# Kernel optimization log

Measured on AMD Instinct MI355X. Metric: run time of the kernel, lower is better.

## Reference

```python
import jax, jax.numpy as jnp
import numpy as np

# dims: channels=512, kernel_size=1, stride=1
B, N, D = 8, 4096, 512
G, GC = 32, 16          # involution groups = D // 16, group_channels = 16
RED = D // 4            # involution reduction_ratio = 4
HID = int(D * 0.25) + 1 # CondConv attention hidden = int(in_planes*0.25)+1 = 129
K = 4                   # number of dynamic-conv experts
TEMP = 34.0             # CondConv softmax temperature
EPS = 1e-5


def setup_inputs() -> dict:
    key = jax.random.key(0)
    ks = jax.random.split(key, 6)
    sc = lambda k, shape, fan: jax.random.normal(k, shape, jnp.float32) / np.float32(np.sqrt(fan))
    return {
        "x": jax.random.normal(ks[0], (B, N, D), jnp.float32),
        # involution: 1x1 conv D->RED (no bias), eval-mode BN, 1x1 conv RED->G (k^2*groups with k=1)
        "conv1_w": sc(ks[1], (RED, D), D),
        "bn_gamma": jnp.ones((RED,), jnp.float32),
        "bn_beta": jnp.zeros((RED,), jnp.float32),
        "bn_mean": jnp.zeros((RED,), jnp.float32),
        "bn_var": jnp.ones((RED,), jnp.float32),
        "conv2_w": sc(ks[2], (G, RED), RED),
        "conv2_b": jnp.zeros((G,), jnp.float32),
        # Dynamic_conv1d (CondConv): attention MLP + K expert 1x1 kernels [K, out, in]
        "fc1_w": sc(ks[3], (HID, D), D),
        "fc2_w": sc(ks[4], (K, HID), HID),
        "fc2_b": jnp.zeros((K,), jnp.float32),
        "dyn_w": sc(ks[5], (K, D, D), D),
        "dyn_b": jnp.zeros((K, D), jnp.float32),
        # LayerNorm(channels)
        "ln_gamma": jnp.ones((D,), jnp.float32),
        "ln_beta": jnp.zeros((D,), jnp.float32),
    }


def reference(x, conv1_w, bn_gamma, bn_beta, bn_mean, bn_var, conv2_w, conv2_b,
              fc1_w, fc2_w, fc2_b, dyn_w, dyn_b, ln_gamma, ln_beta):
    b, n, d = x.shape
    # --- involution branch (k=1, stride=1): per-position, per-group scalar gating ---
    h = jnp.einsum('bnd,rd->bnr', x, conv1_w)                       # 1x1 conv
    h = (h - bn_mean) / jnp.sqrt(bn_var + EPS) * bn_gamma + bn_beta # eval BN
    h = jax.nn.relu(h)
    gate = jnp.einsum('bnr,gr->bng', h, conv2_w) + conv2_b          # [b,n,G] kernel weights (k^2=1)
    out1 = (x.reshape(b, n, G, GC) * gate[..., None]).reshape(b, n, d)
    # --- CondConv dynamic conv1d branch (k=1) ---
    pooled = x.mean(axis=1)                                          # adaptive avg pool over length -> [b,d]
    a = jax.nn.relu(pooled @ fc1_w.T)                                # [b,HID]
    att = jax.nn.softmax((a @ fc2_w.T + fc2_b) / TEMP, axis=-1)      # [b,K]
    Wb = jnp.einsum('bk,kod->bod', att, dyn_w)                       # per-sample kernel [b,d,d]
    bb = att @ dyn_b                                                 # [b,d]
    out2 = jnp.einsum('bnd,bod->bno', x, Wb) + bb[:, None, :]
    # --- LayerNorm + double residual ---
    y = out1 + out2
    mu = y.mean(-1, keepdims=True)
    var = y.var(-1, keepdims=True)
    y = (y - mu) / jnp.sqrt(var + EPS) * ln_gamma + ln_beta
    return y + x
```

## Files before the change

### kernel.cpp

```cpp
#include <hip/hip_runtime.h>

#define DI __device__ __forceinline__

typedef __bf16 bf8 __attribute__((ext_vector_type(8)));
typedef float f4 __attribute__((ext_vector_type(4)));
typedef unsigned short us4 __attribute__((ext_vector_type(4)));
typedef unsigned short us8 __attribute__((ext_vector_type(8)));

#define BB 8
#define NN 4096
#define DD 512
#define RED 128
#define GG 32
#define HID 129

DI float b2f(unsigned short u) {
    union { unsigned int i; float f; } c; c.i = ((unsigned int)u) << 16; return c.f;
}
DI unsigned short f2b(float f) {
    union { float f; unsigned int i; } c; c.f = f;
    unsigned int u = c.i;
    return (unsigned short)((u + 0x7fffu + ((u >> 16) & 1u)) >> 16);
}

typedef const __attribute__((address_space(1))) void* gp1_t;
typedef __attribute__((address_space(3))) void* lp3_t;
DI void gld16(const void* g, void* l) {
    __builtin_amdgcn_global_load_lds((gp1_t)g, (lp3_t)l, 16, 0, 0);
}

__global__ __launch_bounds__(256) void kpre(const float* __restrict__ x,
                                            const float* __restrict__ conv1_w,
                                            const float* __restrict__ conv2_w,
                                            float* __restrict__ part,
                                            unsigned short* __restrict__ xb,
                                            unsigned short* __restrict__ c1b,
                                            unsigned short* __restrict__ c2b) {
    int c = blockIdx.x, b = blockIdx.y, t = threadIdx.x;
    __shared__ float red[2][512];
    if (c >= 128) {
        int idx = ((c - 128) * 8 + b) * 256 + t;
        if (idx < 16384) {
            size_t off = (size_t)idx * 4;
            float4 v = *(const float4*)(conv1_w + off);
            us4 o; o[0] = f2b(v.x); o[1] = f2b(v.y); o[2] = f2b(v.z); o[3] = f2b(v.w);
            *(us4*)(c1b + off) = o;
        } else if (idx < 17408) {
            size_t off = (size_t)(idx - 16384) * 4;
            float4 v = *(const float4*)(conv2_w + off);
            us4 o; o[0] = f2b(v.x); o[1] = f2b(v.y); o[2] = f2b(v.z); o[3] = f2b(v.w);
            *(us4*)(c2b + off) = o;
        }
        return;
    }
    int rg = t >> 7, cg = t & 127;
    int row0 = c * 32 + rg * 16;
    float4 s = {0.f, 0.f, 0.f, 0.f};
#pragma unroll 4
    for (int i = 0; i < 16; ++i) {
        size_t off = ((size_t)(b * NN + row0 + i) * DD) + cg * 4;
        float4 v = *(const float4*)(x + off);
        s.x += v.x; s.y += v.y; s.z += v.z; s.w += v.w;
        us4 o; o[0] = f2b(v.x); o[1] = f2b(v.y); o[2] = f2b(v.z); o[3] = f2b(v.w);
        *(us4*)(xb + off) = o;
    }
    *(float4*)&red[rg][cg * 4] = s;
    __syncthreads();
    if (t < 128) {
        float4 aa = *(const float4*)&red[0][t * 4];
        float4 bb4 = *(const float4*)&red[1][t * 4];
        float4 o;
        o.x = aa.x + bb4.x; o.y = aa.y + bb4.y;
        o.z = aa.z + bb4.z; o.w = aa.w + bb4.w;
        *(float4*)(part + (size_t)(b * 128 + c) * DD + t * 4) = o;
    }
}

__global__ __launch_bounds__(256, 3) void kgate(
    const unsigned short* __restrict__ xb, const unsigned short* __restrict__ c1b,
    const float* __restrict__ bn_g, const float* __restrict__ bn_b,
    const float* __restrict__ bn_m, const float* __restrict__ bn_v,
    const unsigned short* __restrict__ c2b, const float* __restrict__ conv2_b,
    float* __restrict__ gate) {
    int bid = blockIdx.x;
    int b = bid & 7, mtile = bid >> 3;
    int row0 = mtile * 128;
    int t = threadIdx.x;
    int w = t >> 6, lane = t & 63, q = lane >> 4, l16 = lane & 15;
    int wr = (w & 1) * 64, wc = (w >> 1) * 64;

    __shared__ unsigned short As[4096], Bs[4096];
    __shared__ unsigned short h_s[128][136];
    __shared__ float bnS[RED], bnT[RED];

    if (t < RED) {
        float sc = bn_g[t] * rsqrtf(bn_v[t] + 1e-5f);
        bnS[t] = sc;
        bnT[t] = bn_b[t] - bn_m[t] * sc;
    }

    f4 acc[4][4];
#pragma unroll
    for (int mi = 0; mi < 4; ++mi)
#pragma unroll
        for (int ni = 0; ni < 4; ++ni) acc[mi][ni] = (f4){0.f, 0.f, 0.f, 0.f};

    const unsigned short* abase = xb + ((size_t)(b * NN + row0) * DD);
    const int r1 = t >> 2, k1 = (t & 3) * 8;
    const int r2 = 64 + r1, k2 = k1;
    unsigned short* As1 = &As[(size_t)w * 512];
    unsigned short* As2 = &As[2048 + (size_t)w * 512];
    unsigned short* Bs1 = &Bs[(size_t)w * 512];
    unsigned short* Bs2 = &Bs[2048 + (size_t)w * 512];

    for (int ks = 0; ks < 16; ++ks) {
        __syncthreads();
        int kk = ks * 32;
        gld16(abase + (size_t)r1 * DD + kk + k1, As1);
        gld16(abase + (size_t)r2 * DD + kk + k2, As2);
        gld16(c1b + (size_t)r1 * DD + kk + k1, Bs1);
        gld16(c1b + (size_t)r2 * DD + kk + k2, Bs2);
        __syncthreads();
        bf8 af[4], bv[4];
#pragma unroll
        for (int mi = 0; mi < 4; ++mi) af[mi] = *(const bf8*)&As[(wr + mi * 16 + l16) * 32 + q * 8];
#pragma unroll
        for (int ni = 0; ni < 4; ++ni) bv[ni] = *(const bf8*)&Bs[(wc + ni * 16 + l16) * 32 + q * 8];
#pragma unroll
        for (int ni = 0; ni < 4; ++ni)
#pragma unroll
            for (int mi = 0; mi < 4; ++mi)
                acc[mi][ni] = __builtin_amdgcn_mfma_f32_16x16x32_bf16(af[mi], bv[ni], acc[mi][ni], 0, 0, 0);
    }
    __syncthreads();
#pragma unroll
    for (int ni = 0; ni < 4; ++ni) {
        int hc = wc + ni * 16 + l16;
        float sc = bnS[hc], sh = bnT[hc];
#pragma unroll
        for (int mi = 0; mi < 4; ++mi)
#pragma unroll
            for (int r = 0; r < 4; ++r) {
                int row = wr + mi * 16 + q * 4 + r;
                h_s[row][hc] = f2b(fmaxf(acc[mi][ni][r] * sc + sh, 0.f));
            }
    }
    __syncthreads();
    f4 a2[2][2];
#pragma unroll
    for (int mi = 0; mi < 2; ++mi)
#pragma unroll
        for (int ni = 0; ni < 2; ++ni) a2[mi][ni] = (f4){0.f, 0.f, 0.f, 0.f};
#pragma unroll
    for (int ks = 0; ks < 4; ++ks) {
        bf8 ah[2], bh[2];
#pragma unroll
        for (int mi = 0; mi < 2; ++mi)
            ah[mi] = *(const bf8*)&h_s[w * 32 + mi * 16 + l16][ks * 32 + q * 8];
#pragma unroll
        for (int ni = 0; ni < 2; ++ni)
            bh[ni] = *(const bf8*)(c2b + (ni * 16 + l16) * RED + ks * 32 + q * 8);
#pragma unroll
        for (int ni = 0; ni < 2; ++ni)
#pragma unroll
            for (int mi = 0; mi < 2; ++mi)
                a2[mi][ni] = __builtin_amdgcn_mfma_f32_16x16x32_bf16(ah[mi], bh[ni], a2[mi][ni], 0, 0, 0);
    }
#pragma unroll
    for (int ni = 0; ni < 2; ++ni) {
        int g = ni * 16 + l16;
        float cb = conv2_b[g];
#pragma unroll
        for (int mi = 0; mi < 2; ++mi)
#pragma unroll
            for (int r = 0; r < 4; ++r) {
                int row = w * 32 + mi * 16 + q * 4 + r;
                gate[((size_t)(b * NN + row0 + row)) * GG + g] = a2[mi][ni][r] + cb;
            }
    }
}

__global__ __launch_bounds__(256) void katt(const float* __restrict__ part,
                                            const float* __restrict__ fc1_w,
                                            const float* __restrict__ fc2_w,
                                            const float* __restrict__ fc2_b,
                                            const float* __restrict__ dyn_b,
                                            float* __restrict__ att, float* __restrict__ bb) {
    int b = blockIdx.x, t = threadIdx.x;
    __shared__ float sh[2][512];
    __shared__ float pooled[512];
    __shared__ float a_s[HID + 3];
    __shared__ float att_s[4];
    {
        int cg = t & 127, half = t >> 7;
        const float* pb = part + ((size_t)b * 128 + half * 64) * DD + cg * 4;
        float4 s = {0.f, 0.f, 0.f, 0.f};
#pragma unroll 8
        for (int r = 0; r < 64; ++r) {
            float4 v = *(const float4*)(pb + (size_t)r * DD);
            s.x += v.x; s.y += v.y; s.z += v.z; s.w += v.w;
        }
        *(float4*)&sh[half][cg * 4] = s;
    }
    __syncthreads();
    if (t < 128) {
        float4 aa = *(const float4*)&sh[0][t * 4];
        float4 bb4 = *(const float4*)&sh[1][t * 4];
        float4 o;
        o.x = (aa.x + bb4.x) * (1.0f / (float)NN);
        o.y = (aa.y + bb4.y) * (1.0f / (float)NN);
        o.z = (aa.z + bb4.z) * (1.0f / (float)NN);
        o.w = (aa.w + bb4.w) * (1.0f / (float)NN);
        *(float4*)&pooled[t * 4] = o;
    }
    __syncthreads();
    int wv = t >> 6, ln = t & 63;
    float pl[8];
    {
        float4 p0 = *(const float4*)&pooled[ln * 8];
        float4 p1 = *(const float4*)&pooled[ln * 8 + 4];
        pl[0] = p0.x; pl[1] = p0.y; pl[2] = p0.z; pl[3] = p0.w;
        pl[4] = p1.x; pl[5] = p1.y; pl[6] = p1.z; pl[7] = p1.w;
    }
    for (int jb = wv * 4; jb < 128; jb += 16) {
        float s4[4];
#pragma unroll
        for (int u = 0; u < 4; ++u) {
            const float* wr = fc1_w + (size_t)(jb + u) * DD + ln * 8;
            float4 w0 = *(const float4*)wr;
            float4 w1 = *(const float4*)(wr + 4);
            s4[u] = w0.x * pl[0] + w0.y * pl[1] + w0.z * pl[2] + w0.w * pl[3] +
                    w1.x * pl[4] + w1.y * pl[5] + w1.z * pl[6] + w1.w * pl[7];
        }
#pragma unroll
        for (int u = 0; u < 4; ++u) {
            float v = s4[u];
#pragma unroll
            for (int off = 32; off >= 1; off >>= 1) v += __shfl_xor(v, off);
            if (ln == 0) a_s[jb + u] = fmaxf(v, 0.f);
        }
    }
    if (wv == 0) {
        const float* wr = fc1_w + (size_t)128 * DD + ln * 8;
        float4 w0 = *(const float4*)wr;
        float4 w1 = *(const float4*)(wr + 4);
        float v = w0.x * pl[0] + w0.y * pl[1] + w0.z * pl[2] + w0.w * pl[3] +
                  w1.x * pl[4] + w1.y * pl[5] + w1.z * pl[6] + w1.w * pl[7];
#pragma unroll
        for (int off = 32; off >= 1; off >>= 1) v += __shfl_xor(v, off);
        if (ln == 0) a_s[128] = fmaxf(v, 0.f);
    }
    __syncthreads();
    {
        float v = 0.f;
        for (int j = ln; j < HID; j += 64) v += a_s[j] * fc2_w[wv * HID + j];
#pragma unroll
        for (int off = 32; off >= 1; off >>= 1) v += __shfl_xor(v, off);
        if (ln == 0) att_s[wv] = (v + fc2_b[wv]) * (1.0f / 34.0f);
    }
    __syncthreads();
    if (t == 0) {
        float lg[4], mx = -1e30f;
#pragma unroll
        for (int k = 0; k < 4; ++k) { lg[k] = att_s[k]; mx = fmaxf(mx, lg[k]); }
        float den = 0.f;
#pragma unroll
        for (int k = 0; k < 4; ++k) { lg[k] = __expf(lg[k] - mx); den += lg[k]; }
#pragma unroll
        for (int k = 0; k < 4; ++k) {
            float a = lg[k] / den;
            att_s[k] = a; att[b * 4 + k] = a;
        }
    }
    __syncthreads();
    float a0 = att_s[0], a1 = att_s[1], a2 = att_s[2], a3 = att_s[3];
    for (int o = t; o < DD; o += 256) {
        bb[b * DD + o] = a0 * dyn_b[o] + a1 * dyn_b[DD + o] +
                         a2 * dyn_b[2 * DD + o] + a3 * dyn_b[3 * DD + o];
    }
}

__global__ __launch_bounds__(256) void kwb(const float* __restrict__ dyn_w,
                                           const float* __restrict__ att,
                                           unsigned short* __restrict__ Wb) {
    int g = blockIdx.x * 256 + threadIdx.x;
    size_t pos = (size_t)g * 4;
    float4 w0 = *(const float4*)(dyn_w + pos);
    float4 w1 = *(const float4*)(dyn_w + 262144 + pos);
    float4 w2 = *(const float4*)(dyn_w + 524288 + pos);
    float4 w3 = *(const float4*)(dyn_w + 786432 + pos);
#pragma unroll
    for (int b = 0; b < 8; ++b) {
        float a0 = att[b * 4 + 0], a1 = att[b * 4 + 1], a2 = att[b * 4 + 2], a3 = att[b * 4 + 3];
        us4 o;
        o[0] = f2b(a0 * w0.x + a1 * w1.x + a2 * w2.x + a3 * w3.x);
        o[1] = f2b(a0 * w0.y + a1 * w1.y + a2 * w2.y + a3 * w3.y);
        o[2] = f2b(a0 * w0.z + a1 * w1.z + a2 * w2.z + a3 * w3.z);
        o[3] = f2b(a0 * w0.w + a1 * w1.w + a2 * w2.w + a3 * w3.w);
        *(us4*)(Wb + (size_t)b * 262144 + pos) = o;
    }
}

__global__ __launch_bounds__(256, 3) void kgemm(
    const unsigned short* __restrict__ xb, const unsigned short* __restrict__ Wb,
    const float* __restrict__ bb, float* __restrict__ out) {
    int bid = blockIdx.x;
    int b = bid & 7, tile = bid >> 3;
    int ntile = tile & 3, mtile = tile >> 2;
    int row0 = mtile * 128, col0 = ntile * 128;
    int t = threadIdx.x;
    int w = t >> 6, lane = t & 63, q = lane >> 4, l16 = lane & 15;
    int wr = (w & 1) * 64, wc = (w >> 1) * 64;

    __shared__ unsigned short As[4096], Bs[4096];

    f4 acc[4][4];
#pragma unroll
    for (int mi = 0; mi < 4; ++mi)
#pragma unroll
        for (int ni = 0; ni < 4; ++ni) acc[mi][ni] = (f4){0.f, 0.f, 0.f, 0.f};

    const unsigned short* abase = xb + ((size_t)(b * NN + row0) * DD);
    const unsigned short* bbase = Wb + ((size_t)(b * DD + col0)) * DD;
    const int r1 = t >> 2, k1 = (t & 3) * 8;
    const int r2 = 64 + r1;
    unsigned short* As1 = &As[(size_t)w * 512];
    unsigned short* As2 = &As[2048 + (size_t)w * 512];
    unsigned short* Bs1 = &Bs[(size_t)w * 512];
    unsigned short* Bs2 = &Bs[2048 + (size_t)w * 512];

    for (int ks = 0; ks < 16; ++ks) {
        __syncthreads();
        int kk = ks * 32;
        gld16(abase + (size_t)r1 * DD + kk + k1, As1);
        gld16(abase + (size_t)r2 * DD + kk + k1, As2);
        gld16(bbase + (size_t)r1 * DD + kk + k1, Bs1);
        gld16(bbase + (size_t)r2 * DD + kk + k1, Bs2);
        __syncthreads();
        bf8 af[4], bv[4];
#pragma unroll
        for (int mi = 0; mi < 4; ++mi) af[mi] = *(const bf8*)&As[(wr + mi * 16 + l16) * 32 + q * 8];
#pragma unroll
        for (int ni = 0; ni < 4; ++ni) bv[ni] = *(const bf8*)&Bs[(wc + ni * 16 + l16) * 32 + q * 8];
#pragma unroll
        for (int ni = 0; ni < 4; ++ni)
#pragma unroll
            for (int mi = 0; mi < 4; ++mi)
                acc[mi][ni] = __builtin_amdgcn_mfma_f32_16x16x32_bf16(af[mi], bv[ni], acc[mi][ni], 0, 0, 0);
    }
    const float* bbp = bb + b * DD + col0;
#pragma unroll
    for (int ni = 0; ni < 4; ++ni) {
        int col = wc + ni * 16 + l16;
        float bbv = bbp[col];
#pragma unroll
        for (int mi = 0; mi < 4; ++mi)
#pragma unroll
            for (int r = 0; r < 4; ++r) {
                int row = wr + mi * 16 + q * 4 + r;
                out[((size_t)(b * NN + row0 + row)) * DD + col0 + col] = acc[mi][ni][r] + bbv;
            }
    }
}

__global__ __launch_bounds__(256) void kln(const unsigned short* __restrict__ xb,
                                           const float* __restrict__ gate,
                                           const float* __restrict__ lnG,
                                           const float* __restrict__ lnB,
                                           float* __restrict__ out) {
    int t = threadIdx.x;
    int w = t >> 6, lane = t & 63;
    int rid = blockIdx.x * 4 + w;
    size_t base = (size_t)rid * DD + lane * 8;
    float4 y0 = *(const float4*)(out + base);
    float4 y1 = *(const float4*)(out + base + 4);
    us8 xv8 = *(const us8*)(xb + base);
    float g = gate[(size_t)rid * GG + (lane >> 1)];
    float xv[8], y[8];
#pragma unroll
    for (int i = 0; i < 8; ++i) xv[i] = b2f(xv8[i]);
    y[0] = y0.x + xv[0] * g; y[1] = y0.y + xv[1] * g;
    y[2] = y0.z + xv[2] * g; y[3] = y0.w + xv[3] * g;
    y[4] = y1.x + xv[4] * g; y[5] = y1.y + xv[5] * g;
    y[6] = y1.z + xv[6] * g; y[7] = y1.w + xv[7] * g;
    float s = 0.f, sq = 0.f;
#pragma unroll
    for (int i = 0; i < 8; ++i) { s += y[i]; sq += y[i] * y[i]; }
#pragma unroll
    for (int off = 32; off >= 1; off >>= 1) {
        s += __shfl_xor(s, off);
        sq += __shfl_xor(sq, off);
    }
    float mu = s * (1.f / 512.f);
    float rs = rsqrtf(sq * (1.f / 512.f) - mu * mu + 1e-5f);
    float4 g0 = *(const float4*)(lnG + lane * 8);
    float4 g1 = *(const float4*)(lnG + lane * 8 + 4);
    float4 b0 = *(const float4*)(lnB + lane * 8);
    float4 b1 = *(const float4*)(lnB + lane * 8 + 4);
    float lg[8] = {g0.x, g0.y, g0.z, g0.w, g1.x, g1.y, g1.z, g1.w};
    float lb[8] = {b0.x, b0.y, b0.z, b0.w, b1.x, b1.y, b1.z, b1.w};
    float4 o0, o1;
    o0.x = (y[0] - mu) * rs * lg[0] + lb[0] + xv[0];
    o0.y = (y[1] - mu) * rs * lg[1] + lb[1] + xv[1];
    o0.z = (y[2] - mu) * rs * lg[2] + lb[2] + xv[2];
    o0.w = (y[3] - mu) * rs * lg[3] + lb[3] + xv[3];
    o1.x = (y[4] - mu) * rs * lg[4] + lb[4] + xv[4];
    o1.y = (y[5] - mu) * rs * lg[5] + lb[5] + xv[5];
    o1.z = (y[6] - mu) * rs * lg[6] + lb[6] + xv[6];
    o1.w = (y[7] - mu) * rs * lg[7] + lb[7] + xv[7];
    *(float4*)(out + base) = o0;
    *(float4*)(out + base + 4) = o1;
}

extern "C" void kernel_launch(void* const* d_in, const int* in_sizes, int n_in,
                              void* d_out, int out_size, void* d_ws, size_t ws_size,
                              hipStream_t stream) {
    const float* x       = (const float*)d_in[0];
    const float* conv1_w = (const float*)d_in[1];
    const float* bn_g    = (const float*)d_in[2];
    const float* bn_b    = (const float*)d_in[3];
    const float* bn_m    = (const float*)d_in[4];
    const float* bn_v    = (const float*)d_in[5];
    const float* conv2_w = (const float*)d_in[6];
    const float* conv2_b = (const float*)d_in[7];
    const float* fc1_w   = (const float*)d_in[8];
    const float* fc2_w   = (const float*)d_in[9];
    const float* fc2_b   = (const float*)d_in[10];
    const float* dyn_w   = (const float*)d_in[11];
    const float* dyn_b   = (const float*)d_in[12];
    const float* lnG     = (const float*)d_in[13];
    const float* lnB     = (const float*)d_in[14];
    float* out = (float*)d_out;

    char* ws = (char*)d_ws;
    unsigned short* xb   = (unsigned short*)ws;
    float* part          = (float*)(ws + 33554432);
    float* att           = (float*)(ws + 37748736);
    float* bbw           = (float*)(ws + 37748864);
    unsigned short* c1b  = (unsigned short*)(ws + 37765248);
    unsigned short* c2b  = (unsigned short*)(ws + 37896320);
    float* gate          = (float*)(ws + 37904512);
    unsigned short* Wb   = (unsigned short*)(ws + 42098816);

    kpre<<<dim3(137, 8), 256, 0, stream>>>(x, conv1_w, conv2_w, part, xb, c1b, c2b);
    kgate<<<256, 256, 0, stream>>>(xb, c1b, bn_g, bn_b, bn_m, bn_v, c2b, conv2_b, gate);
    katt<<<8, 256, 0, stream>>>(part, fc1_w, fc2_w, fc2_b, dyn_b, att, bbw);
    kwb<<<256, 256, 0, stream>>>(dyn_w, att, Wb);
    kgemm<<<1024, 256, 0, stream>>>(xb, Wb, bbw, out);
    kln<<<8192, 256, 0, stream>>>(xb, gate, lnG, lnB, out);
}
```

Measured before the change: 231.5 us.

## Fuse dynamic-conv GEMM with gating and LayerNorm epilogue in one kernel

```diff
diff --git a/kernel.cpp b/kernel.cpp
--- a/kernel.cpp
+++ b/kernel.cpp
@@ -301,115 +301,136 @@
     }
 }
 
-__global__ __launch_bounds__(256, 3) void kgemm(
+#define STG_BUF 36864
+__global__ __launch_bounds__(512, 2) void kfuse(
     const unsigned short* __restrict__ xb, const unsigned short* __restrict__ Wb,
-    const float* __restrict__ bb, float* __restrict__ out) {
+    const float* __restrict__ bb, const float* __restrict__ gate,
+    const float* __restrict__ lnG, const float* __restrict__ lnB,
+    float* __restrict__ out) {
     int bid = blockIdx.x;
-    int b = bid & 7, tile = bid >> 3;
-    int ntile = tile & 3, mtile = tile >> 2;
-    int row0 = mtile * 128, col0 = ntile * 128;
+    int b = bid & 7, mtile = bid >> 3;
+    int row0 = mtile * 64;
     int t = threadIdx.x;
     int w = t >> 6, lane = t & 63, q = lane >> 4, l16 = lane & 15;
-    int wr = (w & 1) * 64, wc = (w >> 1) * 64;
-
-    __shared__ unsigned short As[4096], Bs[4096];
-
-    f4 acc[4][4];
-#pragma unroll
-    for (int mi = 0; mi < 4; ++mi)
-#pragma unroll
-        for (int ni = 0; ni < 4; ++ni) acc[mi][ni] = (f4){0.f, 0.f, 0.f, 0.f};
+    int wrow = (w >> 2) * 32, wcol = (w & 3) * 128;
+
+    __shared__ __align__(16) char smem[84480];
+    float* gateS = (float*)(smem + 73728);
+    float2* redS = (float2*)(smem + 81920);
+    float2* murs = (float2*)(smem + 83968);
 
     const unsigned short* abase = xb + ((size_t)(b * NN + row0) * DD);
-    const unsigned short* bbase = Wb + ((size_t)(b * DD + col0)) * DD;
-    const int r1 = t >> 2, k1 = (t & 3) * 8;
-    const int r2 = 64 + r1;
-    unsigned short* As1 = &As[(size_t)w * 512];
-    unsigned short* As2 = &As[2048 + (size_t)w * 512];
-    unsigned short* Bs1 = &Bs[(size_t)w * 512];
-    unsigned short* Bs2 = &Bs[2048 + (size_t)w * 512];
-
+    const unsigned short* wbase = Wb + ((size_t)b * DD) * DD;
+
+    {
+        int grow = t >> 3, gcol = (t & 7) * 4;
+        *(float4*)&gateS[t * 4] =
+            *(const float4*)(gate + ((size_t)(b * NN + row0 + grow)) * GG + gcol);
+    }
+
+    const int srow = lane >> 2, skoff = (lane & 3) * 8;
+
+#define STAGE(bf, kk) do {                                                                  \
+        unsigned short* Ab = (unsigned short*)(smem + (bf) * STG_BUF);                      \
+        unsigned short* Bb = (unsigned short*)(smem + (bf) * STG_BUF + 4096);               \
+        if (w < 4)                                                                          \
+            gld16(abase + (size_t)(w * 16 + srow) * DD + (kk) + skoff, Ab + w * 512);       \
+        _Pragma("unroll")                                                                   \
+        for (int i_ = 0; i_ < 4; ++i_)                                                      \
+            gld16(wbase + (size_t)((w * 4 + i_) * 16 + srow) * DD + (kk) + skoff,           \
+                  Bb + (w * 4 + i_) * 512);                                                 \
+    } while (0)
+
+    f4 acc[2][8];
+#pragma unroll
+    for (int mi = 0; mi < 2; ++mi)
+#pragma unroll
+        for (int ni = 0; ni < 8; ++ni) acc[mi][ni] = (f4){0.f, 0.f, 0.f, 0.f};
+
+    STAGE(0, 0);
+    __syncthreads();
     for (int ks = 0; ks < 16; ++ks) {
+        if (ks < 15) STAGE((ks + 1) & 1, (ks + 1) * 32);
+        const unsigned short* A = (const unsigned short*)(smem + (ks & 1) * STG_BUF);
+        const unsigned short* B = (const unsigned short*)(smem + (ks & 1) * STG_BUF + 4096);
+        bf8 af[2], bv[8];
+#pragma unroll
+        for (int mi = 0; mi < 2; ++mi) af[mi] = *(const bf8*)&A[(wrow + mi * 16 + l16) * 32 + q * 8];
+#pragma unroll
+        for (int ni = 0; ni < 8; ++ni) bv[ni] = *(const bf8*)&B[(wcol + ni * 16 + l16) * 32 + q * 8];
+#pragma unroll
+        for (int ni = 0; ni < 8; ++ni)
+#pragma unroll
+            for (int mi = 0; mi < 2; ++mi)
+                acc[mi][ni] = __builtin_amdgcn_mfma_f32_16x16x32_bf16(af[mi], bv[ni], acc[mi][ni], 0, 0, 0);
         __syncthreads();
-        int kk = ks * 32;
-        gld16(abase + (size_t)r1 * DD + kk + k1, As1);
-        gld16(abase + (size_t)r2 * DD + kk + k1, As2);
-        gld16(bbase + (size_t)r1 * DD + kk + k1, Bs1);
-        gld16(bbase + (size_t)r2 * DD + kk + k1, Bs2);
-        __syncthreads();
-        bf8 af[4], bv[4];
-#pragma unroll
-        for (int mi = 0; mi < 4; ++mi) af[mi] = *(const bf8*)&As[(wr + mi * 16 + l16) * 32 + q * 8];
-#pragma unroll
-        for (int ni = 0; ni < 4; ++ni) bv[ni] = *(const bf8*)&Bs[(wc + ni * 16 + l16) * 32 + q * 8];
-#pragma unroll
-        for (int ni = 0; ni < 4; ++ni)
-#pragma unroll
-            for (int mi = 0; mi < 4; ++mi)
-                acc[mi][ni] = __builtin_amdgcn_mfma_f32_16x16x32_bf16(af[mi], bv[ni], acc[mi][ni], 0, 0, 0);
-    }
-    const float* bbp = bb + b * DD + col0;
-#pragma unroll
-    for (int ni = 0; ni < 4; ++ni) {
-        int col = wc + ni * 16 + l16;
-        float bbv = bbp[col];
-#pragma unroll
-        for (int mi = 0; mi < 4; ++mi)
-#pragma unroll
-            for (int r = 0; r < 4; ++r) {
-                int row = wr + mi * 16 + q * 4 + r;
-                out[((size_t)(b * NN + row0 + row)) * DD + col0 + col] = acc[mi][ni][r] + bbv;
+    }
+
+    unsigned short* xs = (unsigned short*)smem;
+#pragma unroll
+    for (int i = 0; i < 8; ++i) {
+        int row = w * 8 + i;
+        gld16(abase + (size_t)row * DD + lane * 8, xs + row * DD);
+    }
+    float bbv[8], lgv[8], lbv[8];
+#pragma unroll
+    for (int ni = 0; ni < 8; ++ni) {
+        int col = wcol + ni * 16 + l16;
+        bbv[ni] = bb[b * DD + col];
+        lgv[ni] = lnG[col];
+        lbv[ni] = lnB[col];
+    }
+    __syncthreads();
+
+    int g0 = wcol >> 4;
+#pragma unroll
+    for (int mi = 0; mi < 2; ++mi) {
+#pragma unroll
+        for (int r = 0; r < 4; ++r) {
+            int row = wrow + mi * 16 + q * 4 + r;
+            float s = 0.f, sq = 0.f;
+#pragma unroll
+            for (int ni = 0; ni < 8; ++ni) {
+                int col = wcol + ni * 16 + l16;
+                float xv = b2f(xs[row * DD + col]);
+                float y = acc[mi][ni][r] + bbv[ni] + xv * gateS[row * GG + g0 + ni];
+                acc[mi][ni][r] = y;
+                s += y; sq += y * y;
             }
-    }
-}
-
-__global__ __launch_bounds__(256) void kln(const unsigned short* __restrict__ xb,
-                                           const float* __restrict__ gate,
-                                           const float* __restrict__ lnG,
-                                           const float* __restrict__ lnB,
-                                           float* __restrict__ out) {
-    int t = threadIdx.x;
-    int w = t >> 6, lane = t & 63;
-    int rid = blockIdx.x * 4 + w;
-    size_t base = (size_t)rid * DD + lane * 8;
-    float4 y0 = *(const float4*)(out + base);
-    float4 y1 = *(const float4*)(out + base + 4);
-    us8 xv8 = *(const us8*)(xb + base);
-    float g = gate[(size_t)rid * GG + (lane >> 1)];
-    float xv[8], y[8];
-#pragma unroll
-    for (int i = 0; i < 8; ++i) xv[i] = b2f(xv8[i]);
-    y[0] = y0.x + xv[0] * g; y[1] = y0.y + xv[1] * g;
-    y[2] = y0.z + xv[2] * g; y[3] = y0.w + xv[3] * g;
-    y[4] = y1.x + xv[4] * g; y[5] = y1.y + xv[5] * g;
-    y[6] = y1.z + xv[6] * g; y[7] = y1.w + xv[7] * g;
-    float s = 0.f, sq = 0.f;
-#pragma unroll
-    for (int i = 0; i < 8; ++i) { s += y[i]; sq += y[i] * y[i]; }
-#pragma unroll
-    for (int off = 32; off >= 1; off >>= 1) {
-        s += __shfl_xor(s, off);
-        sq += __shfl_xor(sq, off);
-    }
-    float mu = s * (1.f / 512.f);
-    float rs = rsqrtf(sq * (1.f / 512.f) - mu * mu + 1e-5f);
-    float4 g0 = *(const float4*)(lnG + lane * 8);
-    float4 g1 = *(const float4*)(lnG + lane * 8 + 4);
-    float4 b0 = *(const float4*)(lnB + lane * 8);
-    float4 b1 = *(const float4*)(lnB + lane * 8 + 4);
-    float lg[8] = {g0.x, g0.y, g0.z, g0.w, g1.x, g1.y, g1.z, g1.w};
-    float lb[8] = {b0.x, b0.y, b0.z, b0.w, b1.x, b1.y, b1.z, b1.w};
-    float4 o0, o1;
-    o0.x = (y[0] - mu) * rs * lg[0] + lb[0] + xv[0];
-    o0.y = (y[1] - mu) * rs * lg[1] + lb[1] + xv[1];
-    o0.z = (y[2] - mu) * rs * lg[2] + lb[2] + xv[2];
-    o0.w = (y[3] - mu) * rs * lg[3] + lb[3] + xv[3];
-    o1.x = (y[4] - mu) * rs * lg[4] + lb[4] + xv[4];
-    o1.y = (y[5] - mu) * rs * lg[5] + lb[5] + xv[5];
-    o1.z = (y[6] - mu) * rs * lg[6] + lb[6] + xv[6];
-    o1.w = (y[7] - mu) * rs * lg[7] + lb[7] + xv[7];
-    *(float4*)(out + base) = o0;
-    *(float4*)(out + base + 4) = o1;
+#pragma unroll
+            for (int off = 8; off >= 1; off >>= 1) {
+                s += __shfl_xor(s, off);
+                sq += __shfl_xor(sq, off);
+            }
+            if (l16 == 0) redS[row * 4 + (w & 3)] = make_float2(s, sq);
+        }
+    }
+    __syncthreads();
+    if (t < 64) {
+        float2 r0 = redS[t * 4], r1 = redS[t * 4 + 1], r2 = redS[t * 4 + 2], r3 = redS[t * 4 + 3];
+        float s = r0.x + r1.x + r2.x + r3.x;
+        float sq = r0.y + r1.y + r2.y + r3.y;
+        float mu = s * (1.f / 512.f);
+        float rs = rsqrtf(sq * (1.f / 512.f) - mu * mu + 1e-5f);
+        murs[t] = make_float2(mu, rs);
+    }
+    __syncthreads();
+#pragma unroll
+    for (int mi = 0; mi < 2; ++mi) {
+#pragma unroll
+        for (int r = 0; r < 4; ++r) {
+            int row = wrow + mi * 16 + q * 4 + r;
+            float2 mr = murs[row];
+            float* op = out + ((size_t)(b * NN + row0 + row)) * DD;
+#pragma unroll
+            for (int ni = 0; ni < 8; ++ni) {
+                int col = wcol + ni * 16 + l16;
+                float xv = b2f(xs[row * DD + col]);
+                op[col] = (acc[mi][ni][r] - mr.x) * mr.y * lgv[ni] + lbv[ni] + xv;
+            }
+        }
+    }
+#undef STAGE
 }
 
 extern "C" void kernel_launch(void* const* d_in, const int* in_sizes, int n_in,
@@ -446,6 +467,5 @@
     kgate<<<256, 256, 0, stream>>>(xb, c1b, bn_g, bn_b, bn_m, bn_v, c2b, conv2_b, gate);
     katt<<<8, 256, 0, stream>>>(part, fc1_w, fc2_w, fc2_b, dyn_b, att, bbw);
     kwb<<<256, 256, 0, stream>>>(dyn_w, att, Wb);
-    kgemm<<<1024, 256, 0, stream>>>(xb, Wb, bbw, out);
-    kln<<<8192, 256, 0, stream>>>(xb, gate, lnG, lnB, out);
-}
+    kfuse<<<512, 512, 0, stream>>>(xb, Wb, bbw, gate, lnG, lnB, out);
+}
```

Result: faster. 223.4 us (-3.5%).
